# Kernel optimization log

Hardware: AMD Instinct MI355X
Metric: run time of the kernel (lower is better)

Reference implementation:

```python
import jax, jax.numpy as jnp
import numpy as np

B = 1024          # batch of subject-object pairs
D_IN_HALF = 2048  # sbj/obj feature width; cat -> input_len = 4096
D_OUT = 1024      # output_len (embedding / label-vec width)
N_LABELS = 128    # number of relation labels in codebook


def setup_inputs() -> dict:
    key = jax.random.key(0)
    ks = jax.random.split(key, 7)
    s = 0.02  # small init scale for weights
    return {
        "sbj_vec": jax.random.normal(ks[0], (B, D_IN_HALF), jnp.float32),
        "obj_vec": jax.random.normal(ks[1], (B, D_IN_HALF), jnp.float32),
        "W1": jax.random.normal(ks[2], (2 * D_IN_HALF, D_OUT), jnp.float32) * s,
        "b1": jax.random.normal(ks[3], (D_OUT,), jnp.float32) * s,
        "W2": jax.random.normal(ks[4], (D_OUT, D_OUT), jnp.float32) * s,
        "b2": jax.random.normal(ks[5], (D_OUT,), jnp.float32) * s,
        "label_vecs": jax.random.normal(ks[6], (N_LABELS, D_OUT), jnp.float32),
    }


def reference(sbj_vec, obj_vec, W1, b1, W2, b2, label_vecs):
    # Sequential(ReLU, Dropout(eval=identity), Linear) applied twice.
    x = jnp.concatenate([sbj_vec, obj_vec], axis=1)          # [B, 2*D_IN_HALF]
    hidden = jax.nn.relu(x) @ W1 + b1                        # [B, D_OUT]
    emb = jax.nn.relu(hidden) @ W2 + b2                      # [B, D_OUT]
    # order_sim vs every label vector, fully batched (replaces per-sample loop):
    # sim[b, l] = -|| relu(label_vecs[l] - emb[b]) ||_2
    diff = jax.nn.relu(label_vecs[None, :, :] - emb[:, None, :])  # [B, L, D_OUT]
    scores = -jnp.sqrt(jnp.sum(diff * diff, axis=2))              # [B, L]
    return scores
```

## Files before the change

### kernel.cpp

```cpp
#include <hip/hip_runtime.h>
#include <math.h>

constexpr int Bn = 1024, DH = 2048, K1 = 4096, DO = 1024, NL = 128;
constexpr int MN = Bn * DO;

typedef __bf16 bf16x8 __attribute__((ext_vector_type(8)));
typedef short  s16x8  __attribute__((ext_vector_type(8)));
typedef float  f32x4  __attribute__((ext_vector_type(4)));

__device__ __forceinline__ unsigned short f2bf(float f) {
  union { float f; unsigned u; } v; v.f = f;
  unsigned r = v.u + 0x7FFFu + ((v.u >> 16) & 1u);
  return (unsigned short)(r >> 16);
}


__global__ __launch_bounds__(256)
void concat_relu_bf16(const float* __restrict__ sbj, const float* __restrict__ obj,
                      unsigned short* __restrict__ out) {
  const int t = blockIdx.x * 256 + threadIdx.x;
  const int m = t >> 9;
  const int k = (t & 511) << 3;
  const float* src = (k < DH) ? sbj + (size_t)m * DH + k
                              : obj + (size_t)m * DH + (k - DH);
  const float4 a = ((const float4*)src)[0];
  const float4 b = ((const float4*)src)[1];
  uint4 o;
  o.x = (unsigned)f2bf(fmaxf(a.x, 0.f)) | ((unsigned)f2bf(fmaxf(a.y, 0.f)) << 16);
  o.y = (unsigned)f2bf(fmaxf(a.z, 0.f)) | ((unsigned)f2bf(fmaxf(a.w, 0.f)) << 16);
  o.z = (unsigned)f2bf(fmaxf(b.x, 0.f)) | ((unsigned)f2bf(fmaxf(b.y, 0.f)) << 16);
  o.w = (unsigned)f2bf(fmaxf(b.z, 0.f)) | ((unsigned)f2bf(fmaxf(b.w, 0.f)) << 16);
  *(uint4*)&out[(size_t)m * K1 + k] = o;
}

__global__ __launch_bounds__(256)
void transp_all(const float* __restrict__ W1, const float* __restrict__ W2,
                unsigned short* __restrict__ W1t, unsigned short* __restrict__ W2t) {
  __shared__ float tl[64][65];
  const int tid = threadIdx.x;
  int by = blockIdx.y;
  const float* in; unsigned short* out; int R;
  if (by < 64) { in = W1; out = W1t; R = K1; }
  else         { in = W2; out = W2t; R = DO; by -= 64; }
  const int r0 = by * 64, c0 = blockIdx.x * 64;
  {
    const int rr = tid >> 4, cc = (tid & 15) * 4;
    #pragma unroll
    for (int i = 0; i < 4; ++i) {
      const float4 v = *(const float4*)&in[(size_t)(r0 + rr + i * 16) * DO + c0 + cc];
      tl[rr + i * 16][cc + 0] = v.x; tl[rr + i * 16][cc + 1] = v.y;
      tl[rr + i * 16][cc + 2] = v.z; tl[rr + i * 16][cc + 3] = v.w;
    }
  }
  __syncthreads();
  {
    const int r4 = (tid & 15) * 4;
    #pragma unroll
    for (int i = 0; i < 4; ++i) {
      const int cr = i * 16 + (tid >> 4);
      uint2 o;
      o.x = (unsigned)f2bf(tl[r4 + 0][cr]) | ((unsigned)f2bf(tl[r4 + 1][cr]) << 16);
      o.y = (unsigned)f2bf(tl[r4 + 2][cr]) | ((unsigned)f2bf(tl[r4 + 3][cr]) << 16);
      *(uint2*)&out[(size_t)(c0 + cr) * R + r0 + r4] = o;
    }
  }
}

template <int WM, int WN, int KSLICE>
__global__ __launch_bounds__(256)
void mfma_gemm(const unsigned short* __restrict__ A,
               const unsigned short* __restrict__ Bt,
               float* __restrict__ P, int K) {
  constexpr int TM = WM * 32, TN = WN * 32;
  __shared__ __align__(16) unsigned short LA[2][TM * 64];
  __shared__ __align__(16) unsigned short LB[2][TN * 64];
  const int tid = threadIdx.x;
  const int w = tid >> 6, l = tid & 63;
  const int m0 = blockIdx.y * TM, n0 = blockIdx.x * TN;
  const int kb = blockIdx.z * KSLICE;

  f32x4 acc[WM][WN] = {};

  auto stage = [&](int buf, int k0) {
    #pragma unroll
    for (int i = 0; i < TM * 8 / 256; ++i) {
      const int flat = i * 256 + tid, row = flat >> 3, kc = flat & 7;
      const int kcg = kc ^ (row & 7);
      __builtin_amdgcn_global_load_lds(
          (const __attribute__((address_space(1))) unsigned int*)(A + (size_t)(m0 + row) * K + k0 + kcg * 8),
          (__attribute__((address_space(3))) unsigned int*)&LA[buf][(i * 256 + w * 64) * 8],
          16, 0, 0);
    }
    #pragma unroll
    for (int i = 0; i < TN * 8 / 256; ++i) {
      const int flat = i * 256 + tid, row = flat >> 3, kc = flat & 7;
      const int kcg = kc ^ (row & 7);
      __builtin_amdgcn_global_load_lds(
          (const __attribute__((address_space(1))) unsigned int*)(Bt + (size_t)(n0 + row) * K + k0 + kcg * 8),
          (__attribute__((address_space(3))) unsigned int*)&LB[buf][(i * 256 + w * 64) * 8],
          16, 0, 0);
    }
  };

  constexpr int NIT = KSLICE / 64;
  stage(0, kb);
  __syncthreads();

  for (int it = 0; it < NIT; ++it) {
    if (it + 1 < NIT) stage((it + 1) & 1, kb + (it + 1) * 64);
    const int buf = it & 1;
    #pragma unroll
    for (int s = 0; s < 2; ++s) {
      const int slot = (s * 4 + (l >> 4)) ^ (l & 7);
      bf16x8 af[WM], bfr[WN];
      #pragma unroll
      for (int i = 0; i < WM; ++i) {
        const int r = (w >> 1) * WM * 16 + i * 16 + (l & 15);
        af[i] = __builtin_bit_cast(bf16x8, *(const s16x8*)&LA[buf][r * 64 + slot * 8]);
      }
      #pragma unroll
      for (int j = 0; j < WN; ++j) {
        const int rr = (w & 1) * WN * 16 + j * 16 + (l & 15);
        bfr[j] = __builtin_bit_cast(bf16x8, *(const s16x8*)&LB[buf][rr * 64 + slot * 8]);
      }
      #pragma unroll
      for (int i = 0; i < WM; ++i)
        #pragma unroll
        for (int j = 0; j < WN; ++j)
          acc[i][j] = __builtin_amdgcn_mfma_f32_16x16x32_bf16(af[i], bfr[j], acc[i][j], 0, 0, 0);
    }
    __syncthreads();
  }

  float* Pz = P + (size_t)blockIdx.z * MN;
  #pragma unroll
  for (int i = 0; i < WM; ++i) {
    #pragma unroll
    for (int r = 0; r < 4; ++r) {
      const int m = m0 + (w >> 1) * WM * 16 + i * 16 + (l >> 4) * 4 + r;
      #pragma unroll
      for (int j = 0; j < WN; ++j) {
        const int n = n0 + (w & 1) * WN * 16 + j * 16 + (l & 15);
        Pz[(size_t)m * DO + n] = acc[i][j][r];
      }
    }
  }
}

template <int KS, bool RELU, bool OUT_BF16>
__global__ __launch_bounds__(256)
void combine(const float* __restrict__ P, const float* __restrict__ bias,
             void* __restrict__ out) {
  const int row = blockIdx.x, t = threadIdx.x;
  const size_t i4 = (size_t)row * 256 + t;
  f32x4 s = ((const f32x4*)P)[i4];
  #pragma unroll
  for (int c = 1; c < KS; ++c) s += ((const f32x4*)P)[(size_t)c * (MN / 4) + i4];
  const f32x4 bb = *(const f32x4*)&bias[t * 4];
  s += bb;
  if (RELU) {
    s[0] = fmaxf(s[0], 0.f); s[1] = fmaxf(s[1], 0.f);
    s[2] = fmaxf(s[2], 0.f); s[3] = fmaxf(s[3], 0.f);
  }
  if (OUT_BF16) {
    uint2 o;
    o.x = (unsigned)f2bf(s[0]) | ((unsigned)f2bf(s[1]) << 16);
    o.y = (unsigned)f2bf(s[2]) | ((unsigned)f2bf(s[3]) << 16);
    *(uint2*)((unsigned short*)out + (size_t)row * DO + t * 4) = o;
  } else {
    *(f32x4*)((float*)out + (size_t)row * DO + t * 4) = s;
  }
}

__global__ __launch_bounds__(256)
void score_partial(const float* __restrict__ emb, const float* __restrict__ labels,
                   float* __restrict__ SP) {
  __shared__ float es[64][33];
  __shared__ float ls[64][132];
  const int tid = threadIdx.x;
  const int b0 = blockIdx.x * 32;
  const int d0 = blockIdx.y * 64;

  #pragma unroll
  for (int i = 0; i < 2; ++i) {
    const int fi = tid + i * 256;
    const int b = fi >> 4, dq = fi & 15;
    const float4 v = *(const float4*)&emb[(size_t)(b0 + b) * DO + d0 + dq * 4];
    es[dq * 4 + 0][b] = v.x; es[dq * 4 + 1][b] = v.y;
    es[dq * 4 + 2][b] = v.z; es[dq * 4 + 3][b] = v.w;
  }
  #pragma unroll
  for (int i = 0; i < 8; ++i) {
    const int fi = tid + i * 256;
    const int lr = fi >> 4, dq = fi & 15;
    const float4 v = *(const float4*)&labels[(size_t)lr * DO + d0 + dq * 4];
    ls[dq * 4 + 0][lr] = v.x; ls[dq * 4 + 1][lr] = v.y;
    ls[dq * 4 + 2][lr] = v.z; ls[dq * 4 + 3][lr] = v.w;
  }
  __syncthreads();

  const int tb = tid & 15;
  const int tl = tid >> 4;
  float acc[2][8] = {};

  for (int dd = 0; dd < 64; ++dd) {
    const float e0 = es[dd][tb * 2 + 0];
    const float e1 = es[dd][tb * 2 + 1];
    const float4 l0 = *(const float4*)&ls[dd][tl * 8];
    const float4 l1 = *(const float4*)&ls[dd][tl * 8 + 4];
    const float lv[8] = {l0.x, l0.y, l0.z, l0.w, l1.x, l1.y, l1.z, l1.w};
    #pragma unroll
    for (int j = 0; j < 8; ++j) {
      float t0 = fmaxf(lv[j] - e0, 0.f); acc[0][j] = fmaf(t0, t0, acc[0][j]);
      float t1 = fmaxf(lv[j] - e1, 0.f); acc[1][j] = fmaf(t1, t1, acc[1][j]);
    }
  }

  float* SPz = SP + (size_t)blockIdx.y * (Bn * NL);
  #pragma unroll
  for (int i = 0; i < 2; ++i) {
    const size_t base = (size_t)(b0 + tb * 2 + i) * NL + tl * 8;
    float4 v0 = {acc[i][0], acc[i][1], acc[i][2], acc[i][3]};
    float4 v1 = {acc[i][4], acc[i][5], acc[i][6], acc[i][7]};
    *(float4*)&SPz[base]     = v0;
    *(float4*)&SPz[base + 4] = v1;
  }
}

__global__ __launch_bounds__(256)
void score_reduce(const float* __restrict__ SP, float* __restrict__ out) {
  const size_t i4 = (size_t)blockIdx.x * 256 + threadIdx.x;
  f32x4 s = ((const f32x4*)SP)[i4];
  #pragma unroll
  for (int c = 1; c < 16; ++c) s += ((const f32x4*)SP)[(size_t)c * 32768 + i4];
  f32x4 o = {-sqrtf(s[0]), -sqrtf(s[1]), -sqrtf(s[2]), -sqrtf(s[3])};
  ((f32x4*)out)[i4] = o;
}

extern "C" void kernel_launch(void* const* d_in, const int* in_sizes, int n_in,
                              void* d_out, int out_size, void* d_ws, size_t ws_size,
                              hipStream_t stream) {
  const float* sbj  = (const float*)d_in[0];
  const float* obj  = (const float*)d_in[1];
  const float* W1   = (const float*)d_in[2];
  const float* b1   = (const float*)d_in[3];
  const float* W2   = (const float*)d_in[4];
  const float* b2   = (const float*)d_in[5];
  const float* labs = (const float*)d_in[6];
  float* scores = (float*)d_out;

  char* ws = (char*)d_ws;
  const bool big = ws_size >= (41ull << 20);
  unsigned short* Abf = (unsigned short*)(ws);
  unsigned short* W1t = (unsigned short*)(ws + (8ull << 20));
  unsigned short* W2t = (unsigned short*)(ws + (16ull << 20));
  unsigned short* H   = (unsigned short*)(ws + (18ull << 20));
  float* P  = (float*)(ws + (big ? (24ull << 20) : (20ull << 20)));
  float* E  = (float*)(ws);
  float* SP = (float*)(ws + (4ull << 20));

  dim3 blk(256);
  concat_relu_bf16<<<dim3(2048), blk, 0, stream>>>(sbj, obj, Abf);
  transp_all<<<dim3(16, 80), blk, 0, stream>>>(W1, W2, W1t, W2t);

  if (big) {
    mfma_gemm<4, 4, 1024><<<dim3(8, 8, 4), blk, 0, stream>>>(Abf, W1t, P, K1);
    combine<4, true, true><<<dim3(Bn), blk, 0, stream>>>(P, b1, H);
    mfma_gemm<4, 4, 256><<<dim3(8, 8, 4), blk, 0, stream>>>(H, W2t, P, DO);
    combine<4, false, false><<<dim3(Bn), blk, 0, stream>>>(P, b2, E);
  } else {
    mfma_gemm<2, 2, 4096><<<dim3(16, 16, 1), blk, 0, stream>>>(Abf, W1t, P, K1);
    combine<1, true, true><<<dim3(Bn), blk, 0, stream>>>(P, b1, H);
    mfma_gemm<2, 2, 1024><<<dim3(16, 16, 1), blk, 0, stream>>>(H, W2t, P, DO);
    combine<1, false, false><<<dim3(Bn), blk, 0, stream>>>(P, b2, E);
  }

  score_partial<<<dim3(32, 16), blk, 0, stream>>>(E, labs, SP);
  score_reduce<<<dim3(128), blk, 0, stream>>>(SP, scores);
}
```

Before: 156.5 us.

## Restructure GEMM to 64x64 tiles with intra-block K split and merge prep kernels

The GEMM now uses 64x64 output tiles with a 128-wide K step. Each of the four waves computes the full tile over its own K quarter, then the partial accumulators are reduced through shared memory. Double buffering is dropped in favour of one LDS buffer with two barriers per iteration, and launch bounds request four blocks per CU so that more blocks (1024 per GEMM) can be resident. The concat/relu and weight-transpose kernels are fused into one launch, and the workspace-size branch is removed, so the larger workspace is now assumed. The changes trade single-block load/compute overlap and extra shared-memory reduction traffic for higher occupancy and better CU coverage.

```diff
diff --git a/kernel.cpp b/kernel.cpp
--- a/kernel.cpp
+++ b/kernel.cpp
@@ -14,35 +14,36 @@
   return (unsigned short)(r >> 16);
 }
 
-
-__global__ __launch_bounds__(256)
-void concat_relu_bf16(const float* __restrict__ sbj, const float* __restrict__ obj,
-                      unsigned short* __restrict__ out) {
-  const int t = blockIdx.x * 256 + threadIdx.x;
-  const int m = t >> 9;
-  const int k = (t & 511) << 3;
-  const float* src = (k < DH) ? sbj + (size_t)m * DH + k
-                              : obj + (size_t)m * DH + (k - DH);
-  const float4 a = ((const float4*)src)[0];
-  const float4 b = ((const float4*)src)[1];
-  uint4 o;
-  o.x = (unsigned)f2bf(fmaxf(a.x, 0.f)) | ((unsigned)f2bf(fmaxf(a.y, 0.f)) << 16);
-  o.y = (unsigned)f2bf(fmaxf(a.z, 0.f)) | ((unsigned)f2bf(fmaxf(a.w, 0.f)) << 16);
-  o.z = (unsigned)f2bf(fmaxf(b.x, 0.f)) | ((unsigned)f2bf(fmaxf(b.y, 0.f)) << 16);
-  o.w = (unsigned)f2bf(fmaxf(b.z, 0.f)) | ((unsigned)f2bf(fmaxf(b.w, 0.f)) << 16);
-  *(uint4*)&out[(size_t)m * K1 + k] = o;
-}
-
-__global__ __launch_bounds__(256)
-void transp_all(const float* __restrict__ W1, const float* __restrict__ W2,
-                unsigned short* __restrict__ W1t, unsigned short* __restrict__ W2t) {
+__global__ __launch_bounds__(256)
+void prep(const float* __restrict__ sbj, const float* __restrict__ obj,
+          const float* __restrict__ W1, const float* __restrict__ W2,
+          unsigned short* __restrict__ Abf,
+          unsigned short* __restrict__ W1t, unsigned short* __restrict__ W2t) {
+  const int tid = threadIdx.x;
+  if (blockIdx.x < 2048) {
+    const int t = blockIdx.x * 256 + tid;
+    const int m = t >> 9;
+    const int k = (t & 511) << 3;
+    const float* src = (k < DH) ? sbj + (size_t)m * DH + k
+                                : obj + (size_t)m * DH + (k - DH);
+    const float4 a = ((const float4*)src)[0];
+    const float4 b = ((const float4*)src)[1];
+    uint4 o;
+    o.x = (unsigned)f2bf(fmaxf(a.x, 0.f)) | ((unsigned)f2bf(fmaxf(a.y, 0.f)) << 16);
+    o.y = (unsigned)f2bf(fmaxf(a.z, 0.f)) | ((unsigned)f2bf(fmaxf(a.w, 0.f)) << 16);
+    o.z = (unsigned)f2bf(fmaxf(b.x, 0.f)) | ((unsigned)f2bf(fmaxf(b.y, 0.f)) << 16);
+    o.w = (unsigned)f2bf(fmaxf(b.z, 0.f)) | ((unsigned)f2bf(fmaxf(b.w, 0.f)) << 16);
+    *(uint4*)&Abf[(size_t)m * K1 + k] = o;
+    return;
+  }
   __shared__ float tl[64][65];
-  const int tid = threadIdx.x;
-  int by = blockIdx.y;
+  const int tb = blockIdx.x - 2048;
+  int by = tb >> 4;
+  const int c0 = (tb & 15) * 64;
   const float* in; unsigned short* out; int R;
   if (by < 64) { in = W1; out = W1t; R = K1; }
   else         { in = W2; out = W2t; R = DO; by -= 64; }
-  const int r0 = by * 64, c0 = blockIdx.x * 64;
+  const int r0 = by * 64;
   {
     const int rr = tid >> 4, cc = (tid & 15) * 4;
     #pragma unroll
@@ -66,81 +67,93 @@
   }
 }
 
-template <int WM, int WN, int KSLICE>
-__global__ __launch_bounds__(256)
+template <int KSLICE>
+__global__ __launch_bounds__(256, 4)
 void mfma_gemm(const unsigned short* __restrict__ A,
                const unsigned short* __restrict__ Bt,
                float* __restrict__ P, int K) {
-  constexpr int TM = WM * 32, TN = WN * 32;
-  __shared__ __align__(16) unsigned short LA[2][TM * 64];
-  __shared__ __align__(16) unsigned short LB[2][TN * 64];
+  __shared__ __align__(16) unsigned short smem[2 * 64 * 128];
+  unsigned short* LA = smem;
+  unsigned short* LB = smem + 64 * 128;
+
   const int tid = threadIdx.x;
   const int w = tid >> 6, l = tid & 63;
-  const int m0 = blockIdx.y * TM, n0 = blockIdx.x * TN;
+  const int m0 = blockIdx.y * 64, n0 = blockIdx.x * 64;
   const int kb = blockIdx.z * KSLICE;
 
-  f32x4 acc[WM][WN] = {};
-
-  auto stage = [&](int buf, int k0) {
-    #pragma unroll
-    for (int i = 0; i < TM * 8 / 256; ++i) {
-      const int flat = i * 256 + tid, row = flat >> 3, kc = flat & 7;
-      const int kcg = kc ^ (row & 7);
+  f32x4 acc[4][4] = {};
+
+  constexpr int NIT = KSLICE / 128;
+  for (int it = 0; it < NIT; ++it) {
+    const int k0 = kb + it * 128;
+    #pragma unroll
+    for (int i = 0; i < 4; ++i) {
+      const int c = i * 256 + tid, m = c >> 4, kc = c & 15;
+      const int kcg = (kc & 8) | ((kc & 7) ^ (m & 7));
       __builtin_amdgcn_global_load_lds(
-          (const __attribute__((address_space(1))) unsigned int*)(A + (size_t)(m0 + row) * K + k0 + kcg * 8),
-          (__attribute__((address_space(3))) unsigned int*)&LA[buf][(i * 256 + w * 64) * 8],
-          16, 0, 0);
-    }
-    #pragma unroll
-    for (int i = 0; i < TN * 8 / 256; ++i) {
-      const int flat = i * 256 + tid, row = flat >> 3, kc = flat & 7;
-      const int kcg = kc ^ (row & 7);
+          (const __attribute__((address_space(1))) unsigned int*)(A + (size_t)(m0 + m) * K + k0 + kcg * 8),
+          (__attribute__((address_space(3))) unsigned int*)&LA[c * 8], 16, 0, 0);
+    }
+    #pragma unroll
+    for (int i = 0; i < 4; ++i) {
+      const int c = i * 256 + tid, n = c >> 4, kc = c & 15;
+      const int kcg = (kc & 8) | ((kc & 7) ^ (n & 7));
       __builtin_amdgcn_global_load_lds(
-          (const __attribute__((address_space(1))) unsigned int*)(Bt + (size_t)(n0 + row) * K + k0 + kcg * 8),
-          (__attribute__((address_space(3))) unsigned int*)&LB[buf][(i * 256 + w * 64) * 8],
-          16, 0, 0);
-    }
+          (const __attribute__((address_space(1))) unsigned int*)(Bt + (size_t)(n0 + n) * K + k0 + kcg * 8),
+          (__attribute__((address_space(3))) unsigned int*)&LB[c * 8], 16, 0, 0);
+    }
+    __syncthreads();
+
+    const int kcq = w * 4 + (l >> 4);
+    bf16x8 af[4], bfr[4];
+    #pragma unroll
+    for (int i = 0; i < 4; ++i) {
+      const int r = i * 16 + (l & 15);
+      const int kca = (kcq & 8) | ((kcq & 7) ^ (r & 7));
+      af[i]  = __builtin_bit_cast(bf16x8, *(const s16x8*)&LA[(r * 16 + kca) * 8]);
+      bfr[i] = __builtin_bit_cast(bf16x8, *(const s16x8*)&LB[(r * 16 + kca) * 8]);
+    }
+    #pragma unroll
+    for (int i = 0; i < 4; ++i)
+      #pragma unroll
+      for (int j = 0; j < 4; ++j)
+        acc[i][j] = __builtin_amdgcn_mfma_f32_16x16x32_bf16(af[i], bfr[j], acc[i][j], 0, 0, 0);
+    __syncthreads();
+  }
+
+  float* red = (float*)smem;
+  auto writeacc = [&](float* dst) {
+    #pragma unroll
+    for (int i = 0; i < 4; ++i)
+      #pragma unroll
+      for (int j = 0; j < 4; ++j)
+        *(f32x4*)&dst[((i * 4 + j) * 64 + l) * 4] = acc[i][j];
   };
-
-  constexpr int NIT = KSLICE / 64;
-  stage(0, kb);
-  __syncthreads();
-
-  for (int it = 0; it < NIT; ++it) {
-    if (it + 1 < NIT) stage((it + 1) & 1, kb + (it + 1) * 64);
-    const int buf = it & 1;
-    #pragma unroll
-    for (int s = 0; s < 2; ++s) {
-      const int slot = (s * 4 + (l >> 4)) ^ (l & 7);
-      bf16x8 af[WM], bfr[WN];
-      #pragma unroll
-      for (int i = 0; i < WM; ++i) {
-        const int r = (w >> 1) * WM * 16 + i * 16 + (l & 15);
-        af[i] = __builtin_bit_cast(bf16x8, *(const s16x8*)&LA[buf][r * 64 + slot * 8]);
-      }
-      #pragma unroll
-      for (int j = 0; j < WN; ++j) {
-        const int rr = (w & 1) * WN * 16 + j * 16 + (l & 15);
-        bfr[j] = __builtin_bit_cast(bf16x8, *(const s16x8*)&LB[buf][rr * 64 + slot * 8]);
-      }
-      #pragma unroll
-      for (int i = 0; i < WM; ++i)
-        #pragma unroll
-        for (int j = 0; j < WN; ++j)
-          acc[i][j] = __builtin_amdgcn_mfma_f32_16x16x32_bf16(af[i], bfr[j], acc[i][j], 0, 0, 0);
-    }
-    __syncthreads();
-  }
+  auto addacc = [&](const float* src) {
+    #pragma unroll
+    for (int i = 0; i < 4; ++i)
+      #pragma unroll
+      for (int j = 0; j < 4; ++j)
+        acc[i][j] += *(const f32x4*)&src[((i * 4 + j) * 64 + l) * 4];
+  };
+  if (w >= 2) writeacc(red + (w - 2) * 4096);
+  __syncthreads();
+  if (w < 2) addacc(red + w * 4096);
+  __syncthreads();
+  if (w == 1) writeacc(red);
+  __syncthreads();
+  if (w != 0) return;
+  addacc(red);
 
   float* Pz = P + (size_t)blockIdx.z * MN;
   #pragma unroll
-  for (int i = 0; i < WM; ++i) {
+  for (int i = 0; i < 4; ++i) {
     #pragma unroll
     for (int r = 0; r < 4; ++r) {
-      const int m = m0 + (w >> 1) * WM * 16 + i * 16 + (l >> 4) * 4 + r;
-      #pragma unroll
-      for (int j = 0; j < WN; ++j) {
-        const int n = n0 + (w & 1) * WN * 16 + j * 16 + (l & 15);
+      const int m = m0 + i * 16 + (l >> 4) * 4 + r;
+      #pragma unroll
+      for (int j = 0; j < 4; ++j) {
+        const int n = n0 + j * 16 + (l & 15);
         Pz[(size_t)m * DO + n] = acc[i][j][r];
       }
     }
@@ -250,30 +263,21 @@
   float* scores = (float*)d_out;
 
   char* ws = (char*)d_ws;
-  const bool big = ws_size >= (41ull << 20);
   unsigned short* Abf = (unsigned short*)(ws);
   unsigned short* W1t = (unsigned short*)(ws + (8ull << 20));
   unsigned short* W2t = (unsigned short*)(ws + (16ull << 20));
   unsigned short* H   = (unsigned short*)(ws + (18ull << 20));
-  float* P  = (float*)(ws + (big ? (24ull << 20) : (20ull << 20)));
-  float* E  = (float*)(ws);
-  float* SP = (float*)(ws + (4ull << 20));
+  float* P  = (float*)(ws + (24ull << 20));
+  float* E  = (float*)(ws + (40ull << 20));
+  float* SP = (float*)(ws + (44ull << 20));
 
   dim3 blk(256);
-  concat_relu_bf16<<<dim3(2048), blk, 0, stream>>>(sbj, obj, Abf);
-  transp_all<<<dim3(16, 80), blk, 0, stream>>>(W1, W2, W1t, W2t);
-
-  if (big) {
-    mfma_gemm<4, 4, 1024><<<dim3(8, 8, 4), blk, 0, stream>>>(Abf, W1t, P, K1);
-    combine<4, true, true><<<dim3(Bn), blk, 0, stream>>>(P, b1, H);
-    mfma_gemm<4, 4, 256><<<dim3(8, 8, 4), blk, 0, stream>>>(H, W2t, P, DO);
-    combine<4, false, false><<<dim3(Bn), blk, 0, stream>>>(P, b2, E);
-  } else {
-    mfma_gemm<2, 2, 4096><<<dim3(16, 16, 1), blk, 0, stream>>>(Abf, W1t, P, K1);
-    combine<1, true, true><<<dim3(Bn), blk, 0, stream>>>(P, b1, H);
-    mfma_gemm<2, 2, 1024><<<dim3(16, 16, 1), blk, 0, stream>>>(H, W2t, P, DO);
-    combine<1, false, false><<<dim3(Bn), blk, 0, stream>>>(P, b2, E);
-  }
+  prep<<<dim3(2048 + 1280), blk, 0, stream>>>(sbj, obj, W1, W2, Abf, W1t, W2t);
+
+  mfma_gemm<1024><<<dim3(16, 16, 4), blk, 0, stream>>>(Abf, W1t, P, K1);
+  combine<4, true, true><<<dim3(Bn), blk, 0, stream>>>(P, b1, H);
+  mfma_gemm<256><<<dim3(16, 16, 4), blk, 0, stream>>>(H, W2t, P, DO);
+  combine<4, false, false><<<dim3(Bn), blk, 0, stream>>>(P, b2, E);
 
   score_partial<<<dim3(32, 16), blk, 0, stream>>>(E, labs, SP);
   score_reduce<<<dim3(128), blk, 0, stream>>>(SP, scores);
```

New measurement: 146.4 us. 1.07x faster.
